# Performance work log

Measured on AMD Instinct MI355X. Metric: run time of the kernel, lower is better.

Reference implementation:

```python
import jax, jax.numpy as jnp
import numpy as np

B, IN, D = 4096, 2048, 2048
NAMES = ["inpgate", "rec_inpgate", "mem_inpgate", "inp", "rec_inp", "readgate",
         "rec_readgate", "mem_readgate", "decoder", "writegate", "rec_writegate",
         "mem_writegate", "encoder"]


def setup_inputs() -> dict:
    key = jax.random.key(0)
    ks = jax.random.split(key, 1 + len(NAMES))
    inp = {
        "x": jax.random.normal(ks[0], (B, IN), jnp.float32),
        "out0": jnp.zeros((B, D), jnp.float32),   # recurrent output state (reset())
        "mem0": jnp.zeros((B, D), jnp.float32),   # memory state (reset())
    }
    for i, n in enumerate(NAMES):
        inp["w_" + n] = jax.random.normal(ks[1 + i], (D, D), jnp.float32) * 0.02
        inp["b_" + n] = jnp.zeros((D,), jnp.float32)
    return inp


def _lin(v, W, b):
    # torch nn.Linear: y = v @ W.T + b, W is [out, in]
    return v @ W.T + b


def reference(x, out0, mem0,
              w_inpgate, b_inpgate, w_rec_inpgate, b_rec_inpgate,
              w_mem_inpgate, b_mem_inpgate, w_inp, b_inp,
              w_rec_inp, b_rec_inp, w_readgate, b_readgate,
              w_rec_readgate, b_rec_readgate, w_mem_readgate, b_mem_readgate,
              w_decoder, b_decoder, w_writegate, b_writegate,
              w_rec_writegate, b_rec_writegate, w_mem_writegate, b_mem_writegate,
              w_encoder, b_encoder):
    sig = jax.nn.sigmoid
    # input block (note: original uses sigmoid here, not tanh)
    block_inp = sig(_lin(x, w_inp, b_inp) + _lin(out0, w_rec_inp, b_rec_inp))
    inp_gate = sig(_lin(x, w_inpgate, b_inpgate)
                   + _lin(mem0, w_mem_inpgate, b_mem_inpgate)
                   + _lin(out0, w_rec_inpgate, b_rec_inpgate))
    read_gate = sig(_lin(x, w_readgate, b_readgate)
                    + _lin(mem0, w_mem_readgate, b_mem_readgate)
                    + _lin(out0, w_rec_readgate, b_rec_readgate))
    decoded_mem = _lin(read_gate * mem0, w_decoder, b_decoder)
    hidden = decoded_mem + block_inp * inp_gate
    write_gate = sig(_lin(x, w_writegate, b_writegate)
                     + _lin(mem0, w_mem_writegate, b_mem_writegate)
                     + _lin(out0, w_rec_writegate, b_rec_writegate))
    enc = jnp.tanh(_lin(hidden, w_encoder, b_encoder))
    mem = (1.0 - write_gate) * mem0 + write_gate * enc
    # torch forward() returns self.out (== hidden_act); mem is internal state
    return hidden
```

## Files before the change

### kernel.cpp

```cpp
#include <hip/hip_runtime.h>
#include <stdint.h>


typedef short bf16x8 __attribute__((ext_vector_type(8)));
typedef float f32x4 __attribute__((ext_vector_type(4)));

#define AS1(p) ((__attribute__((address_space(1))) void*)(uintptr_t)(p))
#define AS3(p) ((__attribute__((address_space(3))) void*)(uint32_t)(uintptr_t)(p))
#define GLD16(gp, lp) __builtin_amdgcn_global_load_lds(AS1(gp), AS3(lp), 16, 0, 0)

template <bool B> struct BoolC { static constexpr bool value = B; };

__device__ __forceinline__ unsigned short f2bf(float f) {
  union { float f; unsigned u; } c; c.f = f;
  unsigned u = c.u;
  unsigned r = (u + 0x7FFFu + ((u >> 16) & 1u)) >> 16;
  return (unsigned short)r;
}
__device__ __forceinline__ float bf2f(unsigned short h) {
  union { unsigned u; float f; } c; c.u = ((unsigned)h) << 16;
  return c.f;
}
__device__ __forceinline__ float sigf(float x) {
  return 1.0f / (1.0f + __expf(-x));
}

__global__ void init_flags_kernel(int* flags) {
  if (threadIdx.x < 2) flags[threadIdx.x] = 0;
}

struct ConvActArgs {
  const float4* src[3];
  ushort4* dst[3];
  int flagidx[3];
  int n4;
  int* flags;
};

__global__ void conv_acts_kernel(ConvActArgs a) {
  const int arr = blockIdx.y;
  const float4* __restrict__ s = a.src[arr];
  ushort4* __restrict__ d = a.dst[arr];
  unsigned nz = 0;
  for (int i = blockIdx.x * blockDim.x + threadIdx.x; i < a.n4;
       i += gridDim.x * blockDim.x) {
    float4 v = s[i];
    union { float f; unsigned u; } cx, cy, cz, cw;
    cx.f = v.x; cy.f = v.y; cz.f = v.z; cw.f = v.w;
    nz |= cx.u | cy.u | cz.u | cw.u;
    ushort4 o;
    o.x = f2bf(v.x); o.y = f2bf(v.y); o.z = f2bf(v.z); o.w = f2bf(v.w);
    d[i] = o;
  }
  const int fi = a.flagidx[arr];
  if (fi >= 0) {
    if (__any(nz != 0u) && (threadIdx.x & 63) == 0) atomicOr(&a.flags[fi], 1);
  }
}

struct ConvWArgs {
  const float4* src[9];
  ushort4* dst[9];
  int flagidx[9];
  int n4;
  const int* flags;
};

__global__ void conv_weights_kernel(ConvWArgs a) {
  const int arr = blockIdx.y;
  const int fi = a.flagidx[arr];
  if (fi >= 0 && a.flags[fi] == 0) return;
  const float4* __restrict__ s = a.src[arr];
  ushort4* __restrict__ d = a.dst[arr];
  for (int i = blockIdx.x * blockDim.x + threadIdx.x; i < a.n4;
       i += gridDim.x * blockDim.x) {
    float4 v = s[i];
    ushort4 o;
    o.x = f2bf(v.x); o.y = f2bf(v.y); o.z = f2bf(v.z); o.w = f2bf(v.w);
    d[i] = o;
  }
}

struct DualArgs {
  const unsigned short *xb, *o0b, *m0b;
  const unsigned short *Winp, *Wrecinp, *Winpgate, *Wrecinpgate, *Wmeminpgate;
  const float *b_inp, *b_rec_inp, *b_inpgate, *b_rec_inpgate, *b_mem_inpgate;
  const float* b_dec;
  const int* flags;
  unsigned short *u1, *u2;
  float* outF;
};

__global__ void __launch_bounds__(512, 2)
gemm_dual(DualArgs a) {
  __shared__ __attribute__((aligned(16))) unsigned short sA[2][256 * 64];
  __shared__ __attribute__((aligned(16))) unsigned short sB1[2][128 * 64];
  __shared__ __attribute__((aligned(16))) unsigned short sB2[2][128 * 64];

  const int tid = threadIdx.x;
  const int l = tid & 63;
  const int w = tid >> 6;
  const int wm = w >> 2, wn = w & 3;
  const int bm = blockIdx.y, bn = blockIdx.x;

  f32x4 acc1[8][2], acc2[8][2];
#pragma unroll
  for (int i = 0; i < 8; ++i)
#pragma unroll
    for (int j = 0; j < 2; ++j) {
      acc1[i][j] = (f32x4){0.f, 0.f, 0.f, 0.f};
      acc2[i][j] = (f32x4){0.f, 0.f, 0.f, 0.f};
    }

  const int srow = l >> 3;
  const int kchS = (l & 7) ^ srow;
  const long long laneA = ((long long)(bm * 256) + srow) * 2048 + kchS * 8;
  const long long laneB = ((long long)(bn * 128) + srow) * 2048 + kchS * 8;

  auto run_pass = [&](auto dc, const unsigned short* Ap,
                      const unsigned short* W1p, const unsigned short* W2p) {
    constexpr bool DUAL = decltype(dc)::value;
    const unsigned short* ga = Ap + laneA;
    const unsigned short* g1 = DUAL ? (W1p + laneB) : (const unsigned short*)0;
    const unsigned short* g2 = W2p + laneB;

    auto stage = [&](int buf, long long koff) {
#pragma unroll
      for (int ii = 0; ii < 4; ++ii) {
        const int q = w * 4 + ii;
        GLD16(ga + koff + (long long)(q * 8) * 2048, (char*)sA[buf] + q * 1024);
      }
#pragma unroll
      for (int ii = 0; ii < 2; ++ii) {
        const int q = w * 2 + ii;
        if constexpr (DUAL)
          GLD16(g1 + koff + (long long)(q * 8) * 2048, (char*)sB1[buf] + q * 1024);
        GLD16(g2 + koff + (long long)(q * 8) * 2048, (char*)sB2[buf] + q * 1024);
      }
    };

    auto compute = [&](int buf) {
#pragma unroll
      for (int ks = 0; ks < 2; ++ks) {
        bf16x8 af[8], b1f[2], b2f[2];
        const int c = ks * 4 + (l >> 4);
#pragma unroll
        for (int ih = 0; ih < 2; ++ih)
#pragma unroll
          for (int i = 0; i < 4; ++i) {
            const int ra = wm * 128 + ih * 64 + i * 16 + (l & 15);
            af[ih * 4 + i] = *(const bf16x8*)(
                (const char*)sA[buf] + (ra * 128 + ((c ^ (ra & 7)) * 16)));
          }
#pragma unroll
        for (int j = 0; j < 2; ++j) {
          const int rb = wn * 32 + j * 16 + (l & 15);
          if constexpr (DUAL)
            b1f[j] = *(const bf16x8*)(
                (const char*)sB1[buf] + (rb * 128 + ((c ^ (rb & 7)) * 16)));
          b2f[j] = *(const bf16x8*)(
              (const char*)sB2[buf] + (rb * 128 + ((c ^ (rb & 7)) * 16)));
        }
#pragma unroll
        for (int ih = 0; ih < 2; ++ih)
#pragma unroll
          for (int i = 0; i < 4; ++i)
#pragma unroll
            for (int j = 0; j < 2; ++j) {
              if constexpr (DUAL)
                acc1[ih * 4 + i][j] = __builtin_amdgcn_mfma_f32_16x16x32_bf16(
                    af[ih * 4 + i], b1f[j], acc1[ih * 4 + i][j], 0, 0, 0);
              acc2[ih * 4 + i][j] = __builtin_amdgcn_mfma_f32_16x16x32_bf16(
                  af[ih * 4 + i], b2f[j], acc2[ih * 4 + i][j], 0, 0, 0);
            }
      }
    };

    stage(0, 0);

    for (int kt = 0; kt < 31; ++kt) {
      const int cur = kt & 1;
      stage(cur ^ 1, (long long)(kt + 1) * 64);
      if constexpr (DUAL)
        asm volatile("s_waitcnt vmcnt(8)" ::: "memory");
      else
        asm volatile("s_waitcnt vmcnt(6)" ::: "memory");
      __builtin_amdgcn_s_barrier();
      asm volatile("" ::: "memory");
      compute(cur);
      asm volatile("s_waitcnt lgkmcnt(0)" ::: "memory");
      __builtin_amdgcn_s_barrier();
    }

    asm volatile("s_waitcnt vmcnt(0)" ::: "memory");
    __builtin_amdgcn_s_barrier();
    asm volatile("" ::: "memory");
    compute(1);
    asm volatile("s_waitcnt lgkmcnt(0)" ::: "memory");
    __builtin_amdgcn_s_barrier();
  };

  const int f_out0 = a.flags[0];
  const int f_mem0 = a.flags[1];

  run_pass(BoolC<true>{}, a.xb, a.Winp, a.Winpgate);
  if (f_out0) run_pass(BoolC<true>{}, a.o0b, a.Wrecinp, a.Wrecinpgate);
  if (f_mem0) run_pass(BoolC<false>{}, a.m0b, (const unsigned short*)0, a.Wmeminpgate);

  const int colb = bn * 128 + wn * 32;
  const int rowb = bm * 256 + wm * 128;
  const bool fast = (f_mem0 == 0);
#pragma unroll
  for (int j = 0; j < 2; ++j) {
    const int col = colb + j * 16 + (l & 15);
    const float s1 = a.b_inp[col] + a.b_rec_inp[col];
    const float s2 = a.b_inpgate[col] + a.b_rec_inpgate[col] + a.b_mem_inpgate[col];
    const float bd = fast ? a.b_dec[col] : 0.f;
#pragma unroll
    for (int ii = 0; ii < 8; ++ii) {
      const int row0 = rowb + (ii >> 2) * 64 + (ii & 3) * 16 + (l >> 4) * 4;
#pragma unroll
      for (int r = 0; r < 4; ++r) {
        const long long idx = (long long)(row0 + r) * 2048 + col;
        const float u1v = acc1[ii][j][r] + s1;
        const float u2v = acc2[ii][j][r] + s2;
        if (fast) {
          a.outF[idx] = sigf(u1v) * sigf(u2v) + bd;
        } else {
          a.u1[idx] = f2bf(u1v);
          a.u2[idx] = f2bf(u2v);
        }
      }
    }
  }
}

struct Job {
  const unsigned short* A0; const unsigned short* W0; const float* b0;
  const unsigned short* A1; const unsigned short* W1; const float* b1;
  const unsigned short* A2; const unsigned short* W2; const float* b2;
  int f0, f1, f2;
  int npairs;
  int jobf;
  const int* flags;
  const float* add;
  float* outF;
  unsigned short* outH;
};

__global__ void __launch_bounds__(256)
gemm_bt_multi(Job jb) {
  __shared__ __attribute__((aligned(16))) unsigned short sA[128 * 64];
  __shared__ __attribute__((aligned(16))) unsigned short sB[128 * 64];

  if (jb.jobf >= 0 && jb.flags[jb.jobf] == 0) return;

  const int tid = threadIdx.x;
  const int l = tid & 63;
  const int w = tid >> 6;
  const int wm = w >> 1, wn = w & 1;
  const int bm = blockIdx.y, bn = blockIdx.x;

  f32x4 acc[4][4];
#pragma unroll
  for (int i = 0; i < 4; ++i)
#pragma unroll
    for (int j = 0; j < 4; ++j) acc[i][j] = (f32x4){0.f, 0.f, 0.f, 0.f};

  const int srow = l >> 3;
  const int kchS = (l & 7) ^ srow;
  const long long laneA = ((long long)bm * 128 + srow) * 2048 + kchS * 8;
  const long long laneB = ((long long)bn * 128 + srow) * 2048 + kchS * 8;

  auto do_pair = [&](const unsigned short* Ap, const unsigned short* Wp) {
    const unsigned short* ga = Ap + laneA;
    const unsigned short* gb = Wp + laneB;
    for (int kt = 0; kt < 32; ++kt) {
#pragma unroll
      for (int ii = 0; ii < 4; ++ii) {
        const int q = w * 4 + ii;
        GLD16(ga + (long long)(q * 8) * 2048, (char*)sA + q * 1024);
        GLD16(gb + (long long)(q * 8) * 2048, (char*)sB + q * 1024);
      }
      __syncthreads();
#pragma unroll
      for (int ks = 0; ks < 2; ++ks) {
        bf16x8 af[4], bf[4];
        const int c = ks * 4 + (l >> 4);
#pragma unroll
        for (int i = 0; i < 4; ++i) {
          const int ra = wm * 64 + i * 16 + (l & 15);
          const int rb = wn * 64 + i * 16 + (l & 15);
          af[i] = *(const bf16x8*)((const char*)sA + (ra * 128 + ((c ^ (ra & 7)) * 16)));
          bf[i] = *(const bf16x8*)((const char*)sB + (rb * 128 + ((c ^ (rb & 7)) * 16)));
        }
#pragma unroll
        for (int i = 0; i < 4; ++i)
#pragma unroll
          for (int j = 0; j < 4; ++j)
            acc[i][j] = __builtin_amdgcn_mfma_f32_16x16x32_bf16(
                af[i], bf[j], acc[i][j], 0, 0, 0);
      }
      __syncthreads();
      ga += 64;
      gb += 64;
    }
  };

  if (jb.f0 < 0 || jb.flags[jb.f0]) do_pair(jb.A0, jb.W0);
  if (jb.npairs > 1 && (jb.f1 < 0 || jb.flags[jb.f1])) do_pair(jb.A1, jb.W1);
  if (jb.npairs > 2 && (jb.f2 < 0 || jb.flags[jb.f2])) do_pair(jb.A2, jb.W2);

  const int colb = bn * 128 + wn * 64;
  const int rowb = bm * 128 + wm * 64;
#pragma unroll
  for (int j = 0; j < 4; ++j) {
    const int col = colb + j * 16 + (l & 15);
    float bias = 0.f;
    if (jb.b0) bias += jb.b0[col];
    if (jb.npairs > 1 && jb.b1) bias += jb.b1[col];
    if (jb.npairs > 2 && jb.b2) bias += jb.b2[col];
#pragma unroll
    for (int i = 0; i < 4; ++i) {
      const int row0 = rowb + i * 16 + (l >> 4) * 4;
#pragma unroll
      for (int r = 0; r < 4; ++r) {
        const long long idx = (long long)(row0 + r) * 2048 + col;
        float v = acc[i][j][r] + bias;
        if (jb.add) v += jb.add[idx];
        if (jb.outF) jb.outF[idx] = v;
        else jb.outH[idx] = f2bf(v);
      }
    }
  }
}

__global__ void gates_kernel(const ushort4* __restrict__ u1,
                             const ushort4* __restrict__ u2,
                             const ushort4* __restrict__ u3,
                             const float4* __restrict__ mem0,
                             float4* __restrict__ g, ushort4* __restrict__ rg,
                             const int* flags, int n4) {
  if (flags[1] == 0) return;
  int i = blockIdx.x * blockDim.x + threadIdx.x;
  if (i >= n4) return;
  ushort4 a = u1[i], b = u2[i], c = u3[i];
  float4 m = mem0[i];
  float4 go;
  ushort4 ro;
  go.x = sigf(bf2f(a.x)) * sigf(bf2f(b.x)); ro.x = f2bf(sigf(bf2f(c.x)) * m.x);
  go.y = sigf(bf2f(a.y)) * sigf(bf2f(b.y)); ro.y = f2bf(sigf(bf2f(c.y)) * m.y);
  go.z = sigf(bf2f(a.z)) * sigf(bf2f(b.z)); ro.z = f2bf(sigf(bf2f(c.z)) * m.z);
  go.w = sigf(bf2f(a.w)) * sigf(bf2f(b.w)); ro.w = f2bf(sigf(bf2f(c.w)) * m.w);
  g[i] = go;
  rg[i] = ro;
}

extern "C" void kernel_launch(void* const* d_in, const int* in_sizes, int n_in,
                              void* d_out, int out_size, void* d_ws, size_t ws_size,
                              hipStream_t stream) {
  (void)in_sizes; (void)n_in; (void)out_size; (void)ws_size;
  const int Bx = 4096, Dx = 2048;
  const size_t ACT = (size_t)Bx * Dx;
  const size_t WEL = (size_t)Dx * Dx;

  const float* x    = (const float*)d_in[0];
  const float* out0 = (const float*)d_in[1];
  const float* mem0 = (const float*)d_in[2];
  const float* w_inpgate     = (const float*)d_in[3];
  const float* b_inpgate     = (const float*)d_in[4];
  const float* w_rec_inpgate = (const float*)d_in[5];
  const float* b_rec_inpgate = (const float*)d_in[6];
  const float* w_mem_inpgate = (const float*)d_in[7];
  const float* b_mem_inpgate = (const float*)d_in[8];
  const float* w_inp         = (const float*)d_in[9];
  const float* b_inp         = (const float*)d_in[10];
  const float* w_rec_inp     = (const float*)d_in[11];
  const float* b_rec_inp     = (const float*)d_in[12];
  const float* w_readgate    = (const float*)d_in[13];
  const float* b_readgate    = (const float*)d_in[14];
  const float* w_rec_readgate= (const float*)d_in[15];
  const float* b_rec_readgate= (const float*)d_in[16];
  const float* w_mem_readgate= (const float*)d_in[17];
  const float* b_mem_readgate= (const float*)d_in[18];
  const float* w_decoder     = (const float*)d_in[19];
  const float* b_decoder     = (const float*)d_in[20];

  char* ws = (char*)d_ws;
  unsigned short* xb  = (unsigned short*)(ws);
  unsigned short* o0b = xb + ACT;
  unsigned short* m0b = o0b + ACT;
  unsigned short* wb  = m0b + ACT;
  unsigned short* u1 = wb + 9 * WEL;
  unsigned short* u2 = u1 + ACT;
  unsigned short* u3 = u2 + ACT;
  float* g = (float*)(u3 + ACT);
  unsigned short* rg = (unsigned short*)(g + ACT);
  int* flags = (int*)(rg + ACT);

  init_flags_kernel<<<1, 64, 0, stream>>>(flags);

  ConvActArgs aa;
  aa.src[0] = (const float4*)x;    aa.dst[0] = (ushort4*)xb;  aa.flagidx[0] = -1;
  aa.src[1] = (const float4*)out0; aa.dst[1] = (ushort4*)o0b; aa.flagidx[1] = 0;
  aa.src[2] = (const float4*)mem0; aa.dst[2] = (ushort4*)m0b; aa.flagidx[2] = 1;
  aa.n4 = (int)(ACT / 4);
  aa.flags = flags;
  conv_acts_kernel<<<dim3(2048, 3, 1), 256, 0, stream>>>(aa);

  ConvWArgs wa;
  const float* wsrc[9] = {w_inp, w_rec_inp, w_inpgate, w_mem_inpgate,
                          w_rec_inpgate, w_readgate, w_mem_readgate,
                          w_rec_readgate, w_decoder};
  const int wflag[9] = {-1, 0, -1, 1, 0, 1, 1, 0, 1};
  for (int i = 0; i < 9; ++i) {
    wa.src[i] = (const float4*)wsrc[i];
    wa.dst[i] = (ushort4*)(wb + (size_t)i * WEL);
    wa.flagidx[i] = wflag[i];
  }
  wa.n4 = (int)(WEL / 4);
  wa.flags = flags;
  conv_weights_kernel<<<dim3(1024, 9, 1), 256, 0, stream>>>(wa);

  DualArgs da;
  da.xb = xb; da.o0b = o0b; da.m0b = m0b;
  da.Winp = wb + 0 * WEL;      da.Wrecinp = wb + 1 * WEL;
  da.Winpgate = wb + 2 * WEL;  da.Wrecinpgate = wb + 4 * WEL;
  da.Wmeminpgate = wb + 3 * WEL;
  da.b_inp = b_inp; da.b_rec_inp = b_rec_inp;
  da.b_inpgate = b_inpgate; da.b_rec_inpgate = b_rec_inpgate;
  da.b_mem_inpgate = b_mem_inpgate;
  da.b_dec = b_decoder;
  da.flags = flags;
  da.u1 = u1; da.u2 = u2;
  da.outF = (float*)d_out;
  gemm_dual<<<dim3(16, 16, 1), 512, 0, stream>>>(da);

  Job J2 = {};
  J2.A0 = xb;  J2.W0 = wb + 5 * WEL; J2.b0 = b_readgate;      J2.f0 = -1;
  J2.A1 = m0b; J2.W1 = wb + 6 * WEL; J2.b1 = b_mem_readgate;  J2.f1 = 1;
  J2.A2 = o0b; J2.W2 = wb + 7 * WEL; J2.b2 = b_rec_readgate;  J2.f2 = 0;
  J2.npairs = 3; J2.jobf = 1; J2.flags = flags; J2.outH = u3;
  gemm_bt_multi<<<dim3(16, 32, 1), 256, 0, stream>>>(J2);

  gates_kernel<<<(int)(ACT / 4 + 255) / 256, 256, 0, stream>>>(
      (const ushort4*)u1, (const ushort4*)u2, (const ushort4*)u3,
      (const float4*)mem0, (float4*)g, (ushort4*)rg, flags, (int)(ACT / 4));

  Job JD = {};
  JD.A0 = rg; JD.W0 = wb + 8 * WEL; JD.b0 = b_decoder; JD.f0 = 1;
  JD.npairs = 1; JD.jobf = 1; JD.flags = flags;
  JD.add = g; JD.outF = (float*)d_out;
  gemm_bt_multi<<<dim3(16, 32, 1), 256, 0, stream>>>(JD);
}
```

Baseline: 369.2 us.

## Interleave paired gate weights and run a four-phase pipelined 256x256 GEMM tile

A new conversion kernel packs each pair of weight matrices (inp/inpgate and rec_inp/rec_inpgate) into one bf16 buffer, interleaving them in 16-row groups. A single 256-wide B tile then feeds both accumulator sets. The dual GEMM is restructured into four quarter-tile phases per k-step: loads for the next slots are issued between phases, and MFMA bursts are wrapped in s_setprio, to overlap global-to-LDS traffic with compute. The mem pass remaps rows on the fly to read only the gate half. Weight buffer slots are reshuffled to match, and the more complex index math and waitcnt choreography add risk.

```diff
diff --git a/kernel.cpp b/kernel.cpp
--- a/kernel.cpp
+++ b/kernel.cpp
@@ -10,6 +10,7 @@
 #define GLD16(gp, lp) __builtin_amdgcn_global_load_lds(AS1(gp), AS3(lp), 16, 0, 0)
 
 template <bool B> struct BoolC { static constexpr bool value = B; };
+template <int I> struct IntC { static constexpr int value = I; };
 
 __device__ __forceinline__ unsigned short f2bf(float f) {
   union { float f; unsigned u; } c; c.f = f;
@@ -58,10 +59,33 @@
   }
 }
 
+struct ConvPackArgs {
+  const float4* wa[2];
+  const float4* wb[2];
+  ushort4* dst[2];
+  int flagidx[2];
+  const int* flags;
+};
+
+__global__ void conv_pack_kernel(ConvPackArgs a) {
+  const int pair = blockIdx.y;
+  const int fi = a.flagidx[pair];
+  if (fi >= 0 && a.flags[fi] == 0) return;
+  const int i = blockIdx.x * blockDim.x + threadIdx.x;
+  const int pr = i >> 9;
+  const int kc = i & 511;
+  const int row = ((pr >> 5) << 4) | (pr & 15);
+  const float4* __restrict__ s = (pr & 16) ? a.wb[pair] : a.wa[pair];
+  float4 v = s[row * 512 + kc];
+  ushort4 o;
+  o.x = f2bf(v.x); o.y = f2bf(v.y); o.z = f2bf(v.z); o.w = f2bf(v.w);
+  a.dst[pair][i] = o;
+}
+
 struct ConvWArgs {
-  const float4* src[9];
-  ushort4* dst[9];
-  int flagidx[9];
+  const float4* src[5];
+  ushort4* dst[5];
+  int flagidx[5];
   int n4;
   const int* flags;
 };
@@ -83,7 +107,7 @@
 
 struct DualArgs {
   const unsigned short *xb, *o0b, *m0b;
-  const unsigned short *Winp, *Wrecinp, *Winpgate, *Wrecinpgate, *Wmeminpgate;
+  const unsigned short *Wpk0, *Wpk1, *Wmem;
   const float *b_inp, *b_rec_inp, *b_inpgate, *b_rec_inpgate, *b_mem_inpgate;
   const float* b_dec;
   const int* flags;
@@ -92,10 +116,11 @@
 };
 
 __global__ void __launch_bounds__(512, 2)
-gemm_dual(DualArgs a) {
-  __shared__ __attribute__((aligned(16))) unsigned short sA[2][256 * 64];
-  __shared__ __attribute__((aligned(16))) unsigned short sB1[2][128 * 64];
-  __shared__ __attribute__((aligned(16))) unsigned short sB2[2][128 * 64];
+gemm_pk(DualArgs a) {
+  __shared__ __attribute__((aligned(16))) unsigned short sA[2][2][128 * 64];
+  __shared__ __attribute__((aligned(16))) unsigned short sB[2][2][128 * 64];
+
+  constexpr int NT = 32;
 
   const int tid = threadIdx.x;
   const int l = tid & 63;
@@ -103,135 +128,148 @@
   const int wm = w >> 2, wn = w & 3;
   const int bm = blockIdx.y, bn = blockIdx.x;
 
-  f32x4 acc1[8][2], acc2[8][2];
-#pragma unroll
-  for (int i = 0; i < 8; ++i)
-#pragma unroll
-    for (int j = 0; j < 2; ++j) {
-      acc1[i][j] = (f32x4){0.f, 0.f, 0.f, 0.f};
-      acc2[i][j] = (f32x4){0.f, 0.f, 0.f, 0.f};
-    }
+  f32x4 acc[2][2][4][2];
+#pragma unroll
+  for (int qm = 0; qm < 2; ++qm)
+#pragma unroll
+    for (int qn = 0; qn < 2; ++qn)
+#pragma unroll
+      for (int i = 0; i < 4; ++i)
+#pragma unroll
+        for (int j = 0; j < 2; ++j)
+          acc[qm][qn][i][j] = (f32x4){0.f, 0.f, 0.f, 0.f};
 
   const int srow = l >> 3;
   const int kchS = (l & 7) ^ srow;
-  const long long laneA = ((long long)(bm * 256) + srow) * 2048 + kchS * 8;
-  const long long laneB = ((long long)(bn * 128) + srow) * 2048 + kchS * 8;
-
-  auto run_pass = [&](auto dc, const unsigned short* Ap,
-                      const unsigned short* W1p, const unsigned short* W2p) {
-    constexpr bool DUAL = decltype(dc)::value;
-    const unsigned short* ga = Ap + laneA;
-    const unsigned short* g1 = DUAL ? (W1p + laneB) : (const unsigned short*)0;
-    const unsigned short* g2 = W2p + laneB;
-
-    auto stage = [&](int buf, long long koff) {
-#pragma unroll
-      for (int ii = 0; ii < 4; ++ii) {
-        const int q = w * 4 + ii;
-        GLD16(ga + koff + (long long)(q * 8) * 2048, (char*)sA[buf] + q * 1024);
-      }
+
+  auto run_pass = [&](auto dc, const unsigned short* Ap, const unsigned short* Bp) {
+    constexpr bool SINGLE = decltype(dc)::value;
+
+    const unsigned short* ga = Ap + ((long long)(bm * 256) + srow) * 2048 + kchS * 8;
+    const unsigned short* gb = SINGLE ? Bp
+                                      : Bp + ((long long)(bn * 256) + srow) * 2048 + kchS * 8;
+
+    auto stageA = [&](int slot, int h, int t) {
+      if (t >= NT) return;
 #pragma unroll
       for (int ii = 0; ii < 2; ++ii) {
         const int q = w * 2 + ii;
-        if constexpr (DUAL)
-          GLD16(g1 + koff + (long long)(q * 8) * 2048, (char*)sB1[buf] + q * 1024);
-        GLD16(g2 + koff + (long long)(q * 8) * 2048, (char*)sB2[buf] + q * 1024);
+        GLD16(ga + (long long)(h * 128 + q * 8) * 2048 + t * 64,
+              (char*)sA[slot][h] + q * 1024);
       }
     };
-
-    auto compute = [&](int buf) {
+    auto stageB = [&](int slot, int h, int t) {
+      if (t >= NT) return;
+#pragma unroll
+      for (int ii = 0; ii < 2; ++ii) {
+        const int q = w * 2 + ii;
+        if constexpr (SINGLE) {
+          const int pr = bn * 256 + h * 128 + q * 8 + srow;
+          const int rr = ((pr >> 5) << 4) | (pr & 15);
+          GLD16(gb + (long long)rr * 2048 + t * 64 + kchS * 8,
+                (char*)sB[slot][h] + q * 1024);
+        } else {
+          GLD16(gb + (long long)(h * 128 + q * 8) * 2048 + t * 64,
+                (char*)sB[slot][h] + q * 1024);
+        }
+      }
+    };
+
+    auto phase = [&](auto qmC, auto qnC, int slot, auto stagefn, bool vm) {
+      constexpr int QM = decltype(qmC)::value;
+      constexpr int QN = decltype(qnC)::value;
+      bf16x8 af[2][4], bfr[2][2];
 #pragma unroll
       for (int ks = 0; ks < 2; ++ks) {
-        bf16x8 af[8], b1f[2], b2f[2];
         const int c = ks * 4 + (l >> 4);
 #pragma unroll
-        for (int ih = 0; ih < 2; ++ih)
-#pragma unroll
-          for (int i = 0; i < 4; ++i) {
-            const int ra = wm * 128 + ih * 64 + i * 16 + (l & 15);
-            af[ih * 4 + i] = *(const bf16x8*)(
-                (const char*)sA[buf] + (ra * 128 + ((c ^ (ra & 7)) * 16)));
-          }
+        for (int i = 0; i < 4; ++i) {
+          const int ra = wm * 64 + i * 16 + (l & 15);
+          af[ks][i] = *(const bf16x8*)((const char*)sA[slot][QM] +
+                                       (ra * 128 + ((c ^ (ra & 7)) * 16)));
+        }
 #pragma unroll
         for (int j = 0; j < 2; ++j) {
+          if (SINGLE && j == 0) continue;
           const int rb = wn * 32 + j * 16 + (l & 15);
-          if constexpr (DUAL)
-            b1f[j] = *(const bf16x8*)(
-                (const char*)sB1[buf] + (rb * 128 + ((c ^ (rb & 7)) * 16)));
-          b2f[j] = *(const bf16x8*)(
-              (const char*)sB2[buf] + (rb * 128 + ((c ^ (rb & 7)) * 16)));
+          bfr[ks][j] = *(const bf16x8*)((const char*)sB[slot][QN] +
+                                        (rb * 128 + ((c ^ (rb & 7)) * 16)));
         }
-#pragma unroll
-        for (int ih = 0; ih < 2; ++ih)
-#pragma unroll
-          for (int i = 0; i < 4; ++i)
-#pragma unroll
-            for (int j = 0; j < 2; ++j) {
-              if constexpr (DUAL)
-                acc1[ih * 4 + i][j] = __builtin_amdgcn_mfma_f32_16x16x32_bf16(
-                    af[ih * 4 + i], b1f[j], acc1[ih * 4 + i][j], 0, 0, 0);
-              acc2[ih * 4 + i][j] = __builtin_amdgcn_mfma_f32_16x16x32_bf16(
-                  af[ih * 4 + i], b2f[j], acc2[ih * 4 + i][j], 0, 0, 0);
-            }
-      }
-    };
-
-    stage(0, 0);
-
-    for (int kt = 0; kt < 31; ++kt) {
-      const int cur = kt & 1;
-      stage(cur ^ 1, (long long)(kt + 1) * 64);
-      if constexpr (DUAL)
-        asm volatile("s_waitcnt vmcnt(8)" ::: "memory");
-      else
-        asm volatile("s_waitcnt vmcnt(6)" ::: "memory");
+      }
+      stagefn();
       __builtin_amdgcn_s_barrier();
       asm volatile("" ::: "memory");
-      compute(cur);
       asm volatile("s_waitcnt lgkmcnt(0)" ::: "memory");
+      __builtin_amdgcn_s_setprio(1);
+#pragma unroll
+      for (int ks = 0; ks < 2; ++ks)
+#pragma unroll
+        for (int i = 0; i < 4; ++i) {
+          if constexpr (!SINGLE)
+            acc[QM][QN][i][0] = __builtin_amdgcn_mfma_f32_16x16x32_bf16(
+                af[ks][i], bfr[ks][0], acc[QM][QN][i][0], 0, 0, 0);
+          acc[QM][QN][i][1] = __builtin_amdgcn_mfma_f32_16x16x32_bf16(
+              af[ks][i], bfr[ks][1], acc[QM][QN][i][1], 0, 0, 0);
+        }
+      __builtin_amdgcn_s_setprio(0);
+      if (vm) asm volatile("s_waitcnt vmcnt(4)" ::: "memory");
       __builtin_amdgcn_s_barrier();
-    }
-
-    asm volatile("s_waitcnt vmcnt(0)" ::: "memory");
+      asm volatile("" ::: "memory");
+    };
+
+    stageA(0, 0, 0); stageB(0, 0, 0); stageB(0, 1, 0); stageA(0, 1, 0);
+    stageA(1, 0, 1); stageB(1, 0, 1);
+    asm volatile("s_waitcnt vmcnt(4)" ::: "memory");
     __builtin_amdgcn_s_barrier();
     asm volatile("" ::: "memory");
-    compute(1);
-    asm volatile("s_waitcnt lgkmcnt(0)" ::: "memory");
-    __builtin_amdgcn_s_barrier();
+
+    for (int t = 0; t < NT - 1; ++t) {
+      const int slot = t & 1, nslot = slot ^ 1;
+      phase(IntC<0>{}, IntC<0>{}, slot, [&] { stageA(nslot, 1, t + 1); }, false);
+      phase(IntC<0>{}, IntC<1>{}, slot, [&] { stageB(nslot, 1, t + 1); }, false);
+      phase(IntC<1>{}, IntC<0>{}, slot, [&] { stageA(slot, 0, t + 2); }, false);
+      phase(IntC<1>{}, IntC<1>{}, slot, [&] { stageB(slot, 0, t + 2); }, true);
+    }
+
+    asm volatile("s_waitcnt vmcnt(0)" ::: "memory");
+    phase(IntC<0>{}, IntC<0>{}, 1, [] {}, false);
+    phase(IntC<0>{}, IntC<1>{}, 1, [] {}, false);
+    phase(IntC<1>{}, IntC<0>{}, 1, [] {}, false);
+    phase(IntC<1>{}, IntC<1>{}, 1, [] {}, false);
   };
 
   const int f_out0 = a.flags[0];
   const int f_mem0 = a.flags[1];
 
-  run_pass(BoolC<true>{}, a.xb, a.Winp, a.Winpgate);
-  if (f_out0) run_pass(BoolC<true>{}, a.o0b, a.Wrecinp, a.Wrecinpgate);
-  if (f_mem0) run_pass(BoolC<false>{}, a.m0b, (const unsigned short*)0, a.Wmeminpgate);
-
-  const int colb = bn * 128 + wn * 32;
-  const int rowb = bm * 256 + wm * 128;
+  run_pass(BoolC<false>{}, a.xb, a.Wpk0);
+  if (f_out0) run_pass(BoolC<false>{}, a.o0b, a.Wpk1);
+  if (f_mem0) run_pass(BoolC<true>{}, a.m0b, a.Wmem);
+
   const bool fast = (f_mem0 == 0);
 #pragma unroll
-  for (int j = 0; j < 2; ++j) {
-    const int col = colb + j * 16 + (l & 15);
+  for (int qn = 0; qn < 2; ++qn) {
+    const int col = bn * 128 + (qn * 4 + wn) * 16 + (l & 15);
     const float s1 = a.b_inp[col] + a.b_rec_inp[col];
     const float s2 = a.b_inpgate[col] + a.b_rec_inpgate[col] + a.b_mem_inpgate[col];
     const float bd = fast ? a.b_dec[col] : 0.f;
 #pragma unroll
-    for (int ii = 0; ii < 8; ++ii) {
-      const int row0 = rowb + (ii >> 2) * 64 + (ii & 3) * 16 + (l >> 4) * 4;
-#pragma unroll
-      for (int r = 0; r < 4; ++r) {
-        const long long idx = (long long)(row0 + r) * 2048 + col;
-        const float u1v = acc1[ii][j][r] + s1;
-        const float u2v = acc2[ii][j][r] + s2;
-        if (fast) {
-          a.outF[idx] = sigf(u1v) * sigf(u2v) + bd;
-        } else {
-          a.u1[idx] = f2bf(u1v);
-          a.u2[idx] = f2bf(u2v);
+    for (int qm = 0; qm < 2; ++qm)
+#pragma unroll
+      for (int i = 0; i < 4; ++i) {
+        const int row0 = bm * 256 + qm * 128 + wm * 64 + i * 16 + (l >> 4) * 4;
+#pragma unroll
+        for (int r = 0; r < 4; ++r) {
+          const long long idx = (long long)(row0 + r) * 2048 + col;
+          const float u1v = acc[qm][qn][i][0][r] + s1;
+          const float u2v = acc[qm][qn][i][1][r] + s2;
+          if (fast) {
+            a.outF[idx] = sigf(u1v) * sigf(u2v) + bd;
+          } else {
+            a.u1[idx] = f2bf(u1v);
+            a.u2[idx] = f2bf(u2v);
+          }
         }
       }
-    }
   }
 }
 
@@ -408,25 +446,32 @@
   aa.flags = flags;
   conv_acts_kernel<<<dim3(2048, 3, 1), 256, 0, stream>>>(aa);
 
+  ConvPackArgs pa;
+  pa.wa[0] = (const float4*)w_inp;     pa.wb[0] = (const float4*)w_inpgate;
+  pa.dst[0] = (ushort4*)(wb + 0 * WEL); pa.flagidx[0] = -1;
+  pa.wa[1] = (const float4*)w_rec_inp; pa.wb[1] = (const float4*)w_rec_inpgate;
+  pa.dst[1] = (ushort4*)(wb + 2 * WEL); pa.flagidx[1] = 0;
+  pa.flags = flags;
+  conv_pack_kernel<<<dim3(8192, 2, 1), 256, 0, stream>>>(pa);
+
   ConvWArgs wa;
-  const float* wsrc[9] = {w_inp, w_rec_inp, w_inpgate, w_mem_inpgate,
-                          w_rec_inpgate, w_readgate, w_mem_readgate,
+  const float* wsrc[5] = {w_mem_inpgate, w_readgate, w_mem_readgate,
                           w_rec_readgate, w_decoder};
-  const int wflag[9] = {-1, 0, -1, 1, 0, 1, 1, 0, 1};
-  for (int i = 0; i < 9; ++i) {
+  const int wflag[5] = {1, 1, 1, 0, 1};
+  for (int i = 0; i < 5; ++i) {
     wa.src[i] = (const float4*)wsrc[i];
-    wa.dst[i] = (ushort4*)(wb + (size_t)i * WEL);
+    wa.dst[i] = (ushort4*)(wb + (size_t)(4 + i) * WEL);
     wa.flagidx[i] = wflag[i];
   }
   wa.n4 = (int)(WEL / 4);
   wa.flags = flags;
-  conv_weights_kernel<<<dim3(1024, 9, 1), 256, 0, stream>>>(wa);
+  conv_weights_kernel<<<dim3(1024, 5, 1), 256, 0, stream>>>(wa);
 
   DualArgs da;
   da.xb = xb; da.o0b = o0b; da.m0b = m0b;
-  da.Winp = wb + 0 * WEL;      da.Wrecinp = wb + 1 * WEL;
-  da.Winpgate = wb + 2 * WEL;  da.Wrecinpgate = wb + 4 * WEL;
-  da.Wmeminpgate = wb + 3 * WEL;
+  da.Wpk0 = wb + 0 * WEL;
+  da.Wpk1 = wb + 2 * WEL;
+  da.Wmem = wb + 4 * WEL;
   da.b_inp = b_inp; da.b_rec_inp = b_rec_inp;
   da.b_inpgate = b_inpgate; da.b_rec_inpgate = b_rec_inpgate;
   da.b_mem_inpgate = b_mem_inpgate;
@@ -434,7 +479,7 @@
   da.flags = flags;
   da.u1 = u1; da.u2 = u2;
   da.outF = (float*)d_out;
-  gemm_dual<<<dim3(16, 16, 1), 512, 0, stream>>>(da);
+  gemm_pk<<<dim3(16, 16, 1), 512, 0, stream>>>(da);
 
   Job J2 = {};
   J2.A0 = xb;  J2.W0 = wb + 5 * WEL; J2.b0 = b_readgate;      J2.f0 = -1;
```

Result: slower. 377.1 us (+2.1%).

## Restructure dual GEMM to 4 waves with register double-buffered fragments and XCD-aware tile mapping

Applied to the files above, without the earlier changes.

The dual-output GEMM now runs 256 threads (4 waves) per block, and each wave computes a 128x64 tile with twice as many accumulators. LDS fragment reads are software-pipelined into two register sets so the next k-slice's loads overlap the current MFMAs, and the global staging is re-ordered around this. Block indices are remapped so each XCD handles a contiguous 2D patch of tiles, aiming for better L2 reuse. The cost is higher register pressure, since 64 accumulators plus two fragment sets per thread may cause spills or limit occupancy to one block per CU.

```diff
diff --git a/kernel.cpp b/kernel.cpp
--- a/kernel.cpp
+++ b/kernel.cpp
@@ -91,7 +91,7 @@
   float* outF;
 };
 
-__global__ void __launch_bounds__(512, 2)
+__global__ void __launch_bounds__(256, 1)
 gemm_dual(DualArgs a) {
   __shared__ __attribute__((aligned(16))) unsigned short sA[2][256 * 64];
   __shared__ __attribute__((aligned(16))) unsigned short sB1[2][128 * 64];
@@ -100,14 +100,19 @@
   const int tid = threadIdx.x;
   const int l = tid & 63;
   const int w = tid >> 6;
-  const int wm = w >> 2, wn = w & 3;
-  const int bm = blockIdx.y, bn = blockIdx.x;
-
-  f32x4 acc1[8][2], acc2[8][2];
+  const int wm = w >> 1, wn = w & 1;
+
+  const int disp = blockIdx.y * gridDim.x + blockIdx.x;
+  const int xcd = disp & 7;
+  const int slot = disp >> 3;
+  const int bm = ((xcd >> 2) << 3) + (slot >> 2);
+  const int bn = ((xcd & 3) << 2) + (slot & 3);
+
+  f32x4 acc1[8][4], acc2[8][4];
 #pragma unroll
   for (int i = 0; i < 8; ++i)
 #pragma unroll
-    for (int j = 0; j < 2; ++j) {
+    for (int j = 0; j < 4; ++j) {
       acc1[i][j] = (f32x4){0.f, 0.f, 0.f, 0.f};
       acc2[i][j] = (f32x4){0.f, 0.f, 0.f, 0.f};
     }
@@ -116,6 +121,9 @@
   const int kchS = (l & 7) ^ srow;
   const long long laneA = ((long long)(bm * 256) + srow) * 2048 + kchS * 8;
   const long long laneB = ((long long)(bn * 128) + srow) * 2048 + kchS * 8;
+
+  bf16x8 aX[8], b1X[4], b2X[4];
+  bf16x8 aY[8], b1Y[4], b2Y[4];
 
   auto run_pass = [&](auto dc, const unsigned short* Ap,
                       const unsigned short* W1p, const unsigned short* W2p) {
@@ -124,80 +132,90 @@
     const unsigned short* g1 = DUAL ? (W1p + laneB) : (const unsigned short*)0;
     const unsigned short* g2 = W2p + laneB;
 
-    auto stage = [&](int buf, long long koff) {
+    auto stage = [&](int buf, int t) {
+      t &= 31;
+      const long long ko = (long long)t * 64;
+#pragma unroll
+      for (int ii = 0; ii < 8; ++ii) {
+        const int q = w * 8 + ii;
+        GLD16(ga + ko + (long long)(q * 8) * 2048, (char*)sA[buf] + q * 1024);
+      }
 #pragma unroll
       for (int ii = 0; ii < 4; ++ii) {
         const int q = w * 4 + ii;
-        GLD16(ga + koff + (long long)(q * 8) * 2048, (char*)sA[buf] + q * 1024);
-      }
-#pragma unroll
-      for (int ii = 0; ii < 2; ++ii) {
-        const int q = w * 2 + ii;
         if constexpr (DUAL)
-          GLD16(g1 + koff + (long long)(q * 8) * 2048, (char*)sB1[buf] + q * 1024);
-        GLD16(g2 + koff + (long long)(q * 8) * 2048, (char*)sB2[buf] + q * 1024);
+          GLD16(g1 + ko + (long long)(q * 8) * 2048, (char*)sB1[buf] + q * 1024);
+        GLD16(g2 + ko + (long long)(q * 8) * 2048, (char*)sB2[buf] + q * 1024);
       }
     };
 
-    auto compute = [&](int buf) {
-#pragma unroll
-      for (int ks = 0; ks < 2; ++ks) {
-        bf16x8 af[8], b1f[2], b2f[2];
-        const int c = ks * 4 + (l >> 4);
-#pragma unroll
-        for (int ih = 0; ih < 2; ++ih)
-#pragma unroll
-          for (int i = 0; i < 4; ++i) {
-            const int ra = wm * 128 + ih * 64 + i * 16 + (l & 15);
-            af[ih * 4 + i] = *(const bf16x8*)(
-                (const char*)sA[buf] + (ra * 128 + ((c ^ (ra & 7)) * 16)));
-          }
-#pragma unroll
-        for (int j = 0; j < 2; ++j) {
-          const int rb = wn * 32 + j * 16 + (l & 15);
+    auto vmwait = [&]() {
+      if constexpr (DUAL)
+        asm volatile("s_waitcnt vmcnt(16)" ::: "memory");
+      else
+        asm volatile("s_waitcnt vmcnt(12)" ::: "memory");
+    };
+
+    auto readF = [&](bf16x8* af, bf16x8* b1, bf16x8* b2, int buf, int ks) {
+      const int c = ks * 4 + (l >> 4);
+#pragma unroll
+      for (int i = 0; i < 8; ++i) {
+        const int ra = wm * 128 + i * 16 + (l & 15);
+        af[i] = *(const bf16x8*)((const char*)sA[buf] +
+                                 (ra * 128 + ((c ^ (ra & 7)) * 16)));
+      }
+#pragma unroll
+      for (int j = 0; j < 4; ++j) {
+        const int rb = wn * 64 + j * 16 + (l & 15);
+        if constexpr (DUAL)
+          b1[j] = *(const bf16x8*)((const char*)sB1[buf] +
+                                   (rb * 128 + ((c ^ (rb & 7)) * 16)));
+        b2[j] = *(const bf16x8*)((const char*)sB2[buf] +
+                                 (rb * 128 + ((c ^ (rb & 7)) * 16)));
+      }
+    };
+
+    auto mfmaAll = [&](const bf16x8* af, const bf16x8* b1, const bf16x8* b2) {
+#pragma unroll
+      for (int i = 0; i < 8; ++i)
+#pragma unroll
+        for (int j = 0; j < 4; ++j) {
           if constexpr (DUAL)
-            b1f[j] = *(const bf16x8*)(
-                (const char*)sB1[buf] + (rb * 128 + ((c ^ (rb & 7)) * 16)));
-          b2f[j] = *(const bf16x8*)(
-              (const char*)sB2[buf] + (rb * 128 + ((c ^ (rb & 7)) * 16)));
+            acc1[i][j] = __builtin_amdgcn_mfma_f32_16x16x32_bf16(
+                af[i], b1[j], acc1[i][j], 0, 0, 0);
+          acc2[i][j] = __builtin_amdgcn_mfma_f32_16x16x32_bf16(
+              af[i], b2[j], acc2[i][j], 0, 0, 0);
         }
-#pragma unroll
-        for (int ih = 0; ih < 2; ++ih)
-#pragma unroll
-          for (int i = 0; i < 4; ++i)
-#pragma unroll
-            for (int j = 0; j < 2; ++j) {
-              if constexpr (DUAL)
-                acc1[ih * 4 + i][j] = __builtin_amdgcn_mfma_f32_16x16x32_bf16(
-                    af[ih * 4 + i], b1f[j], acc1[ih * 4 + i][j], 0, 0, 0);
-              acc2[ih * 4 + i][j] = __builtin_amdgcn_mfma_f32_16x16x32_bf16(
-                  af[ih * 4 + i], b2f[j], acc2[ih * 4 + i][j], 0, 0, 0);
-            }
-      }
     };
 
     stage(0, 0);
-
-    for (int kt = 0; kt < 31; ++kt) {
-      const int cur = kt & 1;
-      stage(cur ^ 1, (long long)(kt + 1) * 64);
-      if constexpr (DUAL)
-        asm volatile("s_waitcnt vmcnt(8)" ::: "memory");
-      else
-        asm volatile("s_waitcnt vmcnt(6)" ::: "memory");
+    stage(1, 1);
+    vmwait();
+    __builtin_amdgcn_s_barrier();
+    asm volatile("" ::: "memory");
+    readF(aX, b1X, b2X, 0, 0);
+
+    for (int t = 0; t < 31; ++t) {
+      const int cb = t & 1;
+      readF(aY, b1Y, b2Y, cb, 1);
+      mfmaAll(aX, b1X, b2X);
+      asm volatile("s_waitcnt lgkmcnt(0)" ::: "memory");
       __builtin_amdgcn_s_barrier();
       asm volatile("" ::: "memory");
-      compute(cur);
-      asm volatile("s_waitcnt lgkmcnt(0)" ::: "memory");
+      stage(cb, t + 2);
+      vmwait();
       __builtin_amdgcn_s_barrier();
+      asm volatile("" ::: "memory");
+      readF(aX, b1X, b2X, cb ^ 1, 0);
+      mfmaAll(aY, b1Y, b2Y);
     }
 
-    asm volatile("s_waitcnt vmcnt(0)" ::: "memory");
+    readF(aY, b1Y, b2Y, 1, 1);
+    mfmaAll(aX, b1X, b2X);
+    mfmaAll(aY, b1Y, b2Y);
+    asm volatile("s_waitcnt lgkmcnt(0) vmcnt(0)" ::: "memory");
     __builtin_amdgcn_s_barrier();
     asm volatile("" ::: "memory");
-    compute(1);
-    asm volatile("s_waitcnt lgkmcnt(0)" ::: "memory");
-    __builtin_amdgcn_s_barrier();
   };
 
   const int f_out0 = a.flags[0];
@@ -207,23 +225,23 @@
   if (f_out0) run_pass(BoolC<true>{}, a.o0b, a.Wrecinp, a.Wrecinpgate);
   if (f_mem0) run_pass(BoolC<false>{}, a.m0b, (const unsigned short*)0, a.Wmeminpgate);
 
-  const int colb = bn * 128 + wn * 32;
+  const int colb = bn * 128 + wn * 64;
   const int rowb = bm * 256 + wm * 128;
   const bool fast = (f_mem0 == 0);
 #pragma unroll
-  for (int j = 0; j < 2; ++j) {
+  for (int j = 0; j < 4; ++j) {
     const int col = colb + j * 16 + (l & 15);
     const float s1 = a.b_inp[col] + a.b_rec_inp[col];
     const float s2 = a.b_inpgate[col] + a.b_rec_inpgate[col] + a.b_mem_inpgate[col];
     const float bd = fast ? a.b_dec[col] : 0.f;
 #pragma unroll
-    for (int ii = 0; ii < 8; ++ii) {
-      const int row0 = rowb + (ii >> 2) * 64 + (ii & 3) * 16 + (l >> 4) * 4;
+    for (int i = 0; i < 8; ++i) {
+      const int row0 = rowb + i * 16 + (l >> 4) * 4;
 #pragma unroll
       for (int r = 0; r < 4; ++r) {
         const long long idx = (long long)(row0 + r) * 2048 + col;
-        const float u1v = acc1[ii][j][r] + s1;
-        const float u2v = acc2[ii][j][r] + s2;
+        const float u1v = acc1[i][j][r] + s1;
+        const float u2v = acc2[i][j][r] + s2;
         if (fast) {
           a.outF[idx] = sigf(u1v) * sigf(u2v) + bd;
         } else {
@@ -434,7 +452,7 @@
   da.flags = flags;
   da.u1 = u1; da.u2 = u2;
   da.outF = (float*)d_out;
-  gemm_dual<<<dim3(16, 16, 1), 512, 0, stream>>>(da);
+  gemm_dual<<<dim3(16, 16, 1), 256, 0, stream>>>(da);
 
   Job J2 = {};
   J2.A0 = xb;  J2.W0 = wb + 5 * WEL; J2.b0 = b_readgate;      J2.f0 = -1;
```

Result: slower. 398.0 us (+7.8%).
